# Kernel optimization log

Measured on AMD Instinct MI355X. Metric: run time of the kernel, lower is better.

Reference implementation:

```python
import jax, jax.numpy as jnp
import numpy as np

R, N1, N2, D = 4, 4096, 4096, 8


def setup_inputs() -> dict:
    key = jax.random.key(0)
    k1, k2, k3 = jax.random.split(key, 3)
    x1 = jax.random.normal(k1, (R, N1, D), dtype=jnp.float32)
    x2 = jax.random.normal(k2, (R, N2, D), dtype=jnp.float32)
    # learned parameters (init: ones), matching nn.Parameter(torch.ones(...))
    lengthscales = jnp.ones((D, 1), dtype=jnp.float32)
    output_scale = jnp.ones((1,), dtype=jnp.float32)
    return {"x1": x1, "x2": x2, "lengthscales": lengthscales, "output_scale": output_scale}


def reference(x1, x2, lengthscales, output_scale):
    # RBF.K: output_scale^2 * exp(-0.5 * sum_d ((x1 - x2) / lengthscales)^2)
    # Computed via the Gram identity ||a-b||^2 = ||a||^2 + ||b||^2 - 2 a.b
    inv_ls = 1.0 / lengthscales.reshape(-1)          # [D]
    a = x1 * inv_ls                                  # [R, N1, D]
    b = x2 * inv_ls                                  # [R, N2, D]
    aa = jnp.sum(a * a, axis=-1)                     # [R, N1]
    bb = jnp.sum(b * b, axis=-1)                     # [R, N2]
    ab = jnp.einsum('rnd,rmd->rnm', a, b)            # [R, N1, N2]
    sqdist = jnp.maximum(aa[:, :, None] + bb[:, None, :] - 2.0 * ab, 0.0)
    return (output_scale[0] ** 2) * jnp.exp(-0.5 * sqdist)
```

## Files before the change

kernel.cpp:

```cpp
#include <hip/hip_runtime.h>


constexpr int D  = 8;
constexpr int BI = 32;
constexpr int BJ = 256;

typedef float vfloat4 __attribute__((ext_vector_type(4)));

#if __has_builtin(__builtin_amdgcn_exp2f)
#define FAST_EXP2(x) __builtin_amdgcn_exp2f(x)
#else
#define FAST_EXP2(x) __expf((x) * 0.69314718f)
#endif

__global__ __launch_bounds__(256, 6) void rbf_kernel(
    const float* __restrict__ x1, const float* __restrict__ x2,
    const float* __restrict__ ls, const float* __restrict__ osc,
    float* __restrict__ out, int N1, int N2)
{
    __shared__ float sb[D][BJ];
    __shared__ float sbb[BJ];
    __shared__ float sa[BI][D];
    __shared__ float sasq[BI];

    const int r   = blockIdx.z;
    const int i0  = blockIdx.y * BI;
    const int j0  = blockIdx.x * BJ;
    const int tid = threadIdx.x;

    float4 l0 = *reinterpret_cast<const float4*>(ls);
    float4 l1 = *reinterpret_cast<const float4*>(ls + 4);
    float4 inv0, inv1;
    inv0.x = 1.0f / l0.x; inv0.y = 1.0f / l0.y; inv0.z = 1.0f / l0.z; inv0.w = 1.0f / l0.w;
    inv1.x = 1.0f / l1.x; inv1.y = 1.0f / l1.y; inv1.z = 1.0f / l1.z; inv1.w = 1.0f / l1.w;

    {
        const float* src = x2 + ((size_t)r * N2 + j0 + tid) * D;
        float4 v0 = *reinterpret_cast<const float4*>(src);
        float4 v1 = *reinterpret_cast<const float4*>(src + 4);
        v0.x *= inv0.x; v0.y *= inv0.y; v0.z *= inv0.z; v0.w *= inv0.w;
        v1.x *= inv1.x; v1.y *= inv1.y; v1.z *= inv1.z; v1.w *= inv1.w;
        sb[0][tid] = v0.x; sb[1][tid] = v0.y; sb[2][tid] = v0.z; sb[3][tid] = v0.w;
        sb[4][tid] = v1.x; sb[5][tid] = v1.y; sb[6][tid] = v1.z; sb[7][tid] = v1.w;
        sbb[tid] = v0.x*v0.x + v0.y*v0.y + v0.z*v0.z + v0.w*v0.w
                 + v1.x*v1.x + v1.y*v1.y + v1.z*v1.z + v1.w*v1.w;
    }
    if (tid < BI) {
        const float* src = x1 + ((size_t)r * N1 + i0 + tid) * D;
        float4 v0 = *reinterpret_cast<const float4*>(src);
        float4 v1 = *reinterpret_cast<const float4*>(src + 4);
        v0.x *= inv0.x; v0.y *= inv0.y; v0.z *= inv0.z; v0.w *= inv0.w;
        v1.x *= inv1.x; v1.y *= inv1.y; v1.z *= inv1.z; v1.w *= inv1.w;
        *reinterpret_cast<float4*>(&sa[tid][0]) = v0;
        *reinterpret_cast<float4*>(&sa[tid][4]) = v1;
        sasq[tid] = v0.x*v0.x + v0.y*v0.y + v0.z*v0.z + v0.w*v0.w
                  + v1.x*v1.x + v1.y*v1.y + v1.z*v1.z + v1.w*v1.w;
    }
    const float os2   = osc[0] * osc[0];
    const float lg2os = __log2f(os2);
    __syncthreads();

    const int lane = tid & 63;
    const int wv   = tid >> 6;

    float4 bd[D];
#pragma unroll
    for (int d = 0; d < D; ++d)
        bd[d] = *reinterpret_cast<const float4*>(&sb[d][lane * 4]);
    const float4 bb4 = *reinterpret_cast<const float4*>(&sbb[lane * 4]);

    constexpr float L2E  = 1.44269504f;
    constexpr float NH2E = -0.72134752f;

    float* obase = out + ((size_t)r * N1 + i0) * (size_t)N2 + j0 + lane * 4;

#pragma unroll
    for (int ii = 0; ii < 8; ++ii) {
        const int row = wv * 8 + ii;
        const float4 a0  = *reinterpret_cast<const float4*>(&sa[row][0]);
        const float4 a1  = *reinterpret_cast<const float4*>(&sa[row][4]);
        const float  asq = sasq[row];

        float4 ch;
        ch.x = fmaf(asq + bb4.x, NH2E, lg2os);
        ch.y = fmaf(asq + bb4.y, NH2E, lg2os);
        ch.z = fmaf(asq + bb4.z, NH2E, lg2os);
        ch.w = fmaf(asq + bb4.w, NH2E, lg2os);

        float d0 = 0.f, d1 = 0.f, d2 = 0.f, d3 = 0.f;
        const float a[D] = {a0.x, a0.y, a0.z, a0.w, a1.x, a1.y, a1.z, a1.w};
#pragma unroll
        for (int d = 0; d < D; ++d) {
            const float av = a[d];
            d0 = fmaf(av, bd[d].x, d0);
            d1 = fmaf(av, bd[d].y, d1);
            d2 = fmaf(av, bd[d].z, d2);
            d3 = fmaf(av, bd[d].w, d3);
        }
        vfloat4 o;
        o.x = FAST_EXP2(fmaf(d0, L2E, ch.x));
        o.y = FAST_EXP2(fmaf(d1, L2E, ch.y));
        o.z = FAST_EXP2(fmaf(d2, L2E, ch.z));
        o.w = FAST_EXP2(fmaf(d3, L2E, ch.w));
        __builtin_nontemporal_store(o, reinterpret_cast<vfloat4*>(obase + (size_t)row * N2));
    }
}

extern "C" void kernel_launch(void* const* d_in, const int* in_sizes, int n_in,
                              void* d_out, int out_size, void* d_ws, size_t ws_size,
                              hipStream_t stream) {
    (void)in_sizes; (void)n_in; (void)d_ws; (void)ws_size; (void)out_size;
    const float* x1  = (const float*)d_in[0];
    const float* x2  = (const float*)d_in[1];
    const float* ls  = (const float*)d_in[2];
    const float* osc = (const float*)d_in[3];
    float* out = (float*)d_out;

    const int R = 4, N1 = 4096, N2 = 4096;
    dim3 grid(N2 / BJ, N1 / BI, R);
    rbf_kernel<<<grid, dim3(256), 0, stream>>>(x1, x2, ls, osc, out, N1, N2);
}
```

Measured before the change: 48.80 us.

## Double column tile per block, precompute column constants, use plain stores

Each block now covers 512 output columns instead of 256, and each thread handles two float4 column groups per row. The per-column part of the exponent (bb*NH2E + log2 os^2) is computed once and added to a per-row term, which removes a few ALU ops per output. Nontemporal stores are replaced with ordinary float4 stores. This halves the grid and the redundant x1 staging, at the cost of more registers (occupancy hint drops from 6 to 4 blocks) and a different cache behaviour for the 256 MB output write.

```diff
diff --git a/kernel.cpp b/kernel.cpp
--- a/kernel.cpp
+++ b/kernel.cpp
@@ -3,9 +3,7 @@
 
 constexpr int D  = 8;
 constexpr int BI = 32;
-constexpr int BJ = 256;
-
-typedef float vfloat4 __attribute__((ext_vector_type(4)));
+constexpr int BJ = 512;
 
 #if __has_builtin(__builtin_amdgcn_exp2f)
 #define FAST_EXP2(x) __builtin_amdgcn_exp2f(x)
@@ -13,7 +11,7 @@
 #define FAST_EXP2(x) __expf((x) * 0.69314718f)
 #endif
 
-__global__ __launch_bounds__(256, 6) void rbf_kernel(
+__global__ __launch_bounds__(256, 4) void rbf_kernel(
     const float* __restrict__ x1, const float* __restrict__ x2,
     const float* __restrict__ ls, const float* __restrict__ osc,
     float* __restrict__ out, int N1, int N2)
@@ -34,16 +32,18 @@
     inv0.x = 1.0f / l0.x; inv0.y = 1.0f / l0.y; inv0.z = 1.0f / l0.z; inv0.w = 1.0f / l0.w;
     inv1.x = 1.0f / l1.x; inv1.y = 1.0f / l1.y; inv1.z = 1.0f / l1.z; inv1.w = 1.0f / l1.w;
 
-    {
-        const float* src = x2 + ((size_t)r * N2 + j0 + tid) * D;
+#pragma unroll
+    for (int k = 0; k < 2; ++k) {
+        const int p = k * 256 + tid;
+        const float* src = x2 + ((size_t)r * N2 + j0 + p) * D;
         float4 v0 = *reinterpret_cast<const float4*>(src);
         float4 v1 = *reinterpret_cast<const float4*>(src + 4);
         v0.x *= inv0.x; v0.y *= inv0.y; v0.z *= inv0.z; v0.w *= inv0.w;
         v1.x *= inv1.x; v1.y *= inv1.y; v1.z *= inv1.z; v1.w *= inv1.w;
-        sb[0][tid] = v0.x; sb[1][tid] = v0.y; sb[2][tid] = v0.z; sb[3][tid] = v0.w;
-        sb[4][tid] = v1.x; sb[5][tid] = v1.y; sb[6][tid] = v1.z; sb[7][tid] = v1.w;
-        sbb[tid] = v0.x*v0.x + v0.y*v0.y + v0.z*v0.z + v0.w*v0.w
-                 + v1.x*v1.x + v1.y*v1.y + v1.z*v1.z + v1.w*v1.w;
+        sb[0][p] = v0.x; sb[1][p] = v0.y; sb[2][p] = v0.z; sb[3][p] = v0.w;
+        sb[4][p] = v1.x; sb[5][p] = v1.y; sb[6][p] = v1.z; sb[7][p] = v1.w;
+        sbb[p] = v0.x*v0.x + v0.y*v0.y + v0.z*v0.z + v0.w*v0.w
+               + v1.x*v1.x + v1.y*v1.y + v1.z*v1.z + v1.w*v1.w;
     }
     if (tid < BI) {
         const float* src = x1 + ((size_t)r * N1 + i0 + tid) * D;
@@ -63,14 +63,23 @@
     const int lane = tid & 63;
     const int wv   = tid >> 6;
 
-    float4 bd[D];
+    float4 bd0[D], bd1[D];
 #pragma unroll
-    for (int d = 0; d < D; ++d)
-        bd[d] = *reinterpret_cast<const float4*>(&sb[d][lane * 4]);
-    const float4 bb4 = *reinterpret_cast<const float4*>(&sbb[lane * 4]);
+    for (int d = 0; d < D; ++d) {
+        bd0[d] = *reinterpret_cast<const float4*>(&sb[d][lane * 4]);
+        bd1[d] = *reinterpret_cast<const float4*>(&sb[d][256 + lane * 4]);
+    }
+    const float4 bbA = *reinterpret_cast<const float4*>(&sbb[lane * 4]);
+    const float4 bbB = *reinterpret_cast<const float4*>(&sbb[256 + lane * 4]);
 
     constexpr float L2E  = 1.44269504f;
     constexpr float NH2E = -0.72134752f;
+
+    float4 cb0, cb1;
+    cb0.x = fmaf(bbA.x, NH2E, lg2os); cb0.y = fmaf(bbA.y, NH2E, lg2os);
+    cb0.z = fmaf(bbA.z, NH2E, lg2os); cb0.w = fmaf(bbA.w, NH2E, lg2os);
+    cb1.x = fmaf(bbB.x, NH2E, lg2os); cb1.y = fmaf(bbB.y, NH2E, lg2os);
+    cb1.z = fmaf(bbB.z, NH2E, lg2os); cb1.w = fmaf(bbB.w, NH2E, lg2os);
 
     float* obase = out + ((size_t)r * N1 + i0) * (size_t)N2 + j0 + lane * 4;
 
@@ -79,30 +88,35 @@
         const int row = wv * 8 + ii;
         const float4 a0  = *reinterpret_cast<const float4*>(&sa[row][0]);
         const float4 a1  = *reinterpret_cast<const float4*>(&sa[row][4]);
-        const float  asq = sasq[row];
+        const float  ca  = sasq[row] * NH2E;
 
-        float4 ch;
-        ch.x = fmaf(asq + bb4.x, NH2E, lg2os);
-        ch.y = fmaf(asq + bb4.y, NH2E, lg2os);
-        ch.z = fmaf(asq + bb4.z, NH2E, lg2os);
-        ch.w = fmaf(asq + bb4.w, NH2E, lg2os);
-
-        float d0 = 0.f, d1 = 0.f, d2 = 0.f, d3 = 0.f;
+        float p0 = 0.f, p1 = 0.f, p2 = 0.f, p3 = 0.f;
+        float q0 = 0.f, q1 = 0.f, q2 = 0.f, q3 = 0.f;
         const float a[D] = {a0.x, a0.y, a0.z, a0.w, a1.x, a1.y, a1.z, a1.w};
 #pragma unroll
         for (int d = 0; d < D; ++d) {
             const float av = a[d];
-            d0 = fmaf(av, bd[d].x, d0);
-            d1 = fmaf(av, bd[d].y, d1);
-            d2 = fmaf(av, bd[d].z, d2);
-            d3 = fmaf(av, bd[d].w, d3);
+            p0 = fmaf(av, bd0[d].x, p0);
+            p1 = fmaf(av, bd0[d].y, p1);
+            p2 = fmaf(av, bd0[d].z, p2);
+            p3 = fmaf(av, bd0[d].w, p3);
+            q0 = fmaf(av, bd1[d].x, q0);
+            q1 = fmaf(av, bd1[d].y, q1);
+            q2 = fmaf(av, bd1[d].z, q2);
+            q3 = fmaf(av, bd1[d].w, q3);
         }
-        vfloat4 o;
-        o.x = FAST_EXP2(fmaf(d0, L2E, ch.x));
-        o.y = FAST_EXP2(fmaf(d1, L2E, ch.y));
-        o.z = FAST_EXP2(fmaf(d2, L2E, ch.z));
-        o.w = FAST_EXP2(fmaf(d3, L2E, ch.w));
-        __builtin_nontemporal_store(o, reinterpret_cast<vfloat4*>(obase + (size_t)row * N2));
+        float4 oA, oB;
+        oA.x = FAST_EXP2(fmaf(p0, L2E, ca + cb0.x));
+        oA.y = FAST_EXP2(fmaf(p1, L2E, ca + cb0.y));
+        oA.z = FAST_EXP2(fmaf(p2, L2E, ca + cb0.z));
+        oA.w = FAST_EXP2(fmaf(p3, L2E, ca + cb0.w));
+        oB.x = FAST_EXP2(fmaf(q0, L2E, ca + cb1.x));
+        oB.y = FAST_EXP2(fmaf(q1, L2E, ca + cb1.y));
+        oB.z = FAST_EXP2(fmaf(q2, L2E, ca + cb1.z));
+        oB.w = FAST_EXP2(fmaf(q3, L2E, ca + cb1.w));
+        float* op = obase + (size_t)row * N2;
+        *reinterpret_cast<float4*>(op)       = oA;
+        *reinterpret_cast<float4*>(op + 256) = oB;
     }
 }
 
```

Result: faster. 47.54 us (-2.6%).
